# Kernel optimization log

Hardware: AMD Instinct MI355X
Metric: run time of the kernel (lower is better)

The kernel has to match this reference:

```python
import jax, jax.numpy as jnp
import numpy as np
import math

DIM = 1024
HEADS = 16
DIM_HEAD = 64
INNER = HEADS * DIM_HEAD
NUM_BUCKETS = 32
MAX_DISTANCE = 128


def setup_inputs() -> dict:
    key = jax.random.key(0)
    ks = jax.random.split(key, 6)
    x = jax.random.normal(ks[0], (2, 2048, DIM), dtype=jnp.float32)
    Wq = jax.random.normal(ks[1], (DIM, INNER), dtype=jnp.float32) * (DIM ** -0.5)
    Wkv = jax.random.normal(ks[2], (DIM, 2 * DIM_HEAD), dtype=jnp.float32) * (DIM ** -0.5)
    Wout = jax.random.normal(ks[3], (INNER, DIM), dtype=jnp.float32) * (INNER ** -0.5)
    bout = jnp.zeros((DIM,), dtype=jnp.float32)
    rel_emb = jax.random.normal(ks[4], (NUM_BUCKETS, HEADS), dtype=jnp.float32) * 0.02
    return {"x": x, "Wq": Wq, "Wkv": Wkv, "Wout": Wout, "bout": bout, "rel_emb": rel_emb}


def _relative_position_bucket(rel_pos, num_buckets=NUM_BUCKETS, max_distance=MAX_DISTANCE):
    # rel_pos: [i, j] int32, k_pos - q_pos
    n = jnp.maximum(-rel_pos, 0)
    max_exact = num_buckets // 2
    is_small = n < max_exact
    n_safe = jnp.maximum(n, 1)  # avoid log(0); masked by is_small anyway
    val_if_large = max_exact + (
        jnp.log(n_safe.astype(jnp.float32) / max_exact)
        / math.log(max_distance / max_exact)
        * (num_buckets - max_exact)
    ).astype(jnp.int32)
    val_if_large = jnp.minimum(val_if_large, num_buckets - 1)
    return jnp.where(is_small, n, val_if_large)


def reference(x, Wq, Wkv, Wout, bout, rel_emb):
    b, n, _ = x.shape
    scale = DIM_HEAD ** -0.5
    bias_scale = DIM_HEAD ** 0.5

    q = (x @ Wq).reshape(b, n, HEADS, DIM_HEAD).transpose(0, 2, 1, 3) * scale  # [b,h,n,d]
    kv = x @ Wkv  # [b,n,2d]
    k, v = kv[..., :DIM_HEAD], kv[..., DIM_HEAD:]  # shared single-head K/V [b,n,d]

    sim = jnp.einsum('bhid,bjd->bhij', q, k)

    # T5 relative position bias
    pos = jnp.arange(n, dtype=jnp.int32)
    rel_pos = pos[None, :] - pos[:, None]  # [i,j] = k_pos - q_pos
    rp_bucket = _relative_position_bucket(rel_pos)
    bias = rel_emb[rp_bucket]  # [i,j,h]
    sim = sim + jnp.transpose(bias, (2, 0, 1))[None] * bias_scale

    # causal mask: mask strictly-upper triangle
    causal_mask = jnp.triu(jnp.ones((n, n), dtype=bool), k=1)
    neg = jnp.finfo(sim.dtype).max
    sim = jnp.where(causal_mask[None, None], -neg, sim)

    attn = jax.nn.softmax(sim, axis=-1)
    out = jnp.einsum('bhij,bjd->bhid', attn, v)
    out = out.transpose(0, 2, 1, 3).reshape(b, n, INNER)
    return out @ Wout + bout
```

## Files before the change

kernel.cpp:

```cpp
#include <hip/hip_runtime.h>
#include <cstdint>
#include <cmath>

typedef _Float16 half8 __attribute__((ext_vector_type(8)));
typedef unsigned short ushort8 __attribute__((ext_vector_type(8)));
typedef float floatx4 __attribute__((ext_vector_type(4)));

#define VT_STRIDE 2080

__device__ __forceinline__ unsigned short f2h(float f) {
    union { _Float16 h; unsigned short u; } cv;
    cv.h = (_Float16)f;
    return cv.u;
}

__device__ __forceinline__ void gld_lds16(const unsigned short* g, unsigned short* l) {
    __builtin_amdgcn_global_load_lds(
        (const __attribute__((address_space(1))) unsigned int*)g,
        (__attribute__((address_space(3))) unsigned int*)l, 16, 0, 0);
}

__global__ void cast_x_kernel(const float* __restrict__ x, unsigned short* __restrict__ xh, int n8) {
    int idx = blockIdx.x * blockDim.x + threadIdx.x;
    if (idx >= n8) return;
    const float4* p = (const float4*)x;
    float4 a = p[idx * 2], b = p[idx * 2 + 1];
    ushort8 o;
    o[0] = f2h(a.x); o[1] = f2h(a.y); o[2] = f2h(a.z); o[3] = f2h(a.w);
    o[4] = f2h(b.x); o[5] = f2h(b.y); o[6] = f2h(b.z); o[7] = f2h(b.w);
    *(ushort8*)(xh + (size_t)idx * 8) = o;
}

__global__ void transpose_fused_kernel(const float* __restrict__ Wq, const float* __restrict__ Wkv,
                                       const float* __restrict__ Wout,
                                       unsigned short* __restrict__ Wqkvt, unsigned short* __restrict__ Wot) {
    __shared__ float tile[32][33];
    int bxi = blockIdx.x;
    const float* in; unsigned short* out; int C; int cb;
    if (bxi < 32)      { in = Wq;   out = Wqkvt;                 C = 1024; cb = bxi; }
    else if (bxi < 36) { in = Wkv;  out = Wqkvt + 1024 * 1024;   C = 128;  cb = bxi - 32; }
    else               { in = Wout; out = Wot;                   C = 1024; cb = bxi - 36; }
    int bx = cb * 32, by = blockIdx.y * 32;
    int x = threadIdx.x, y0 = threadIdx.y;
    #pragma unroll
    for (int k = 0; k < 4; k++) {
        int y = y0 + k * 8;
        tile[y][x] = in[(size_t)(by + y) * C + bx + x];
    }
    __syncthreads();
    #pragma unroll
    for (int k = 0; k < 4; k++) {
        int y = y0 + k * 8;
        out[(size_t)(bx + y) * 1024 + by + x] = f2h(tile[x][y]);
    }
}

template<int MODE>
__global__ __launch_bounds__(256) void gemm_mn(
    const unsigned short* __restrict__ A, const unsigned short* __restrict__ Bt,
    unsigned short* __restrict__ oq, unsigned short* __restrict__ ok,
    unsigned short* __restrict__ ov, float* __restrict__ of,
    const float* __restrict__ bias)
{
    __shared__ __align__(16) unsigned short As[64 * 40];
    __shared__ __align__(16) unsigned short Bs[128 * 40];
    const int K = 1024;
    int t = threadIdx.x;
    int w = t >> 6, lane = t & 63, g = lane >> 4, il = lane & 15;
    int m0 = blockIdx.y * 64, n0 = blockIdx.x * 128;
    int ar = t >> 2, ac = (t & 3) * 8;
    int br = t >> 1, bc = (t & 1) * 16;
    floatx4 acc[8] = {};
    const unsigned short* Ap = A + (size_t)(m0 + ar) * K + ac;
    const unsigned short* Bp = Bt + (size_t)(n0 + br) * K + bc;
    for (int k0 = 0; k0 < K; k0 += 32) {
        ushort8 av  = *(const ushort8*)(Ap + k0);
        ushort8 bv0 = *(const ushort8*)(Bp + k0);
        ushort8 bv1 = *(const ushort8*)(Bp + k0 + 8);
        __syncthreads();
        *(ushort8*)&As[ar * 40 + ac] = av;
        *(ushort8*)&Bs[br * 40 + bc] = bv0;
        *(ushort8*)&Bs[br * 40 + bc + 8] = bv1;
        __syncthreads();
        half8 af = *(const half8*)&As[(w * 16 + il) * 40 + g * 8];
        #pragma unroll
        for (int nt = 0; nt < 8; nt++) {
            half8 bf = *(const half8*)&Bs[(nt * 16 + il) * 40 + g * 8];
            acc[nt] = __builtin_amdgcn_mfma_f32_16x16x32_f16(af, bf, acc[nt], 0, 0, 0);
        }
    }
    #pragma unroll
    for (int nt = 0; nt < 8; nt++) {
        #pragma unroll
        for (int r = 0; r < 4; r++) {
            int row = m0 + w * 16 + 4 * g + r;
            int col = n0 + nt * 16 + il;
            float v = acc[nt][r];
            if (MODE == 0) {
                if (col < 1024) {
                    int b = row >> 11, i = row & 2047, h = col >> 6, d = col & 63;
                    oq[(size_t)((b * 16 + h) * 2048 + i) * 64 + d] = f2h(v * 0.18033688011112042f);
                } else if (col < 1088) {
                    ok[(size_t)row * 64 + (col - 1024)] = f2h(v);
                } else {
                    int b = row >> 11, j = row & 2047;
                    ov[(size_t)((b << 6) + (col - 1088)) * VT_STRIDE + j] = f2h(v);
                }
            } else {
                of[(size_t)row * 1024 + col] = v + bias[col];
            }
        }
    }
}

__global__ __launch_bounds__(256) void attn_kernel(
    const unsigned short* __restrict__ qh, const unsigned short* __restrict__ kh,
    const unsigned short* __restrict__ vt, const float* __restrict__ rel_emb,
    unsigned short* __restrict__ ob)
{
    __shared__ float bias_tab[256];
    __shared__ __align__(16) unsigned short Ks[2][64 * 64];
    __shared__ __align__(16) unsigned short Vs[64 * 64];
    __shared__ __align__(16) unsigned short Pl[64 * 72];

    int bx = 31 - blockIdx.y;
    int bh = blockIdx.x;
    int b = bh >> 4, h = bh & 15;
    int t = threadIdx.x;
    int w = t >> 6, lane = t & 63, g = lane >> 4, il = lane & 15;

    {
        int dlt = t;
        int bucket;
        if (dlt < 16) bucket = dlt;
        else {
            float lg = logf((float)dlt * 0.0625f) / 2.0794415416798357f;
            int vv = 16 + (int)(lg * 16.0f);
            bucket = vv < 31 ? vv : 31;
        }
        bias_tab[dlt] = rel_emb[bucket * 16 + h] * 11.541560327111708f;
    }
    float cb31 = rel_emb[31 * 16 + h] * 11.541560327111708f;

    const unsigned short* kbase = kh + (size_t)b * (2048 * 64);
    const unsigned short* vbase = vt + (size_t)b * (64 * VT_STRIDE);
    int prow = (w * 16 + il) * 72;

    int l8 = lane >> 3, b8 = lane & 7;
    int swz = (b8 ^ l8) * 8;
    const unsigned short* kg_base = kbase + (size_t)(w * 16 + l8) * 64 + swz;
    const unsigned short* vg_base = vbase + (size_t)(w * 16 + l8) * VT_STRIDE + swz;
    int e0 = (g ^ (il & 7)) * 8;

    int iw = bx * 64 + w * 16;
    int i_glob = iw + il;
    const unsigned short* qrow = qh + (size_t)(bh * 2048 + i_glob) * 64;
    half8 qf0 = *(const half8*)(qrow + g * 8);
    half8 qf1 = *(const half8*)(qrow + 32 + g * 8);
    floatx4 O[4] = {};
    float m_run = -1e30f, l_run = 0.0f;

    gld_lds16(kg_base,                 &Ks[0][(w * 16) * 64]);
    gld_lds16(kg_base + 8 * 64,        &Ks[0][(w * 16 + 8) * 64]);
    gld_lds16(vg_base,                 &Vs[(w * 16) * 64]);
    gld_lds16(vg_base + 8 * VT_STRIDE, &Vs[(w * 16 + 8) * 64]);

    for (int c = 0; c <= bx; c++) {
        __syncthreads();
        if (c < bx) {
            const unsigned short* kg = kg_base + (size_t)(c + 1) * 4096;
            unsigned short* kd = &Ks[(c + 1) & 1][0];
            gld_lds16(kg,          &kd[(w * 16) * 64]);
            gld_lds16(kg + 8 * 64, &kd[(w * 16 + 8) * 64]);
        }
        const unsigned short* Kc = &Ks[c & 1][0];
        int j0 = c * 64;

        floatx4 S[4] = {};
        #pragma unroll
        for (int jt = 0; jt < 4; jt++) {
            half8 k0 = *(const half8*)&Kc[jt * 1024 + il * 64 + e0];
            half8 k1 = *(const half8*)&Kc[jt * 1024 + il * 64 + (e0 ^ 32)];
            S[jt] = __builtin_amdgcn_mfma_f32_16x16x32_f16(k0, qf0, S[jt], 0, 0, 0);
            S[jt] = __builtin_amdgcn_mfma_f32_16x16x32_f16(k1, qf1, S[jt], 0, 0, 0);
        }
        half8 vf[8];
        #pragma unroll
        for (int ks = 0; ks < 2; ks++)
            #pragma unroll
            for (int dt = 0; dt < 4; dt++)
                vf[ks * 4 + dt] = *(const half8*)&Vs[dt * 1024 + il * 64 + (e0 ^ (ks * 32))];

        asm volatile("s_waitcnt lgkmcnt(0)" ::: "memory");
        __builtin_amdgcn_s_barrier();
        if (c < bx) {
            const unsigned short* vg = vg_base + (c + 1) * 64;
            gld_lds16(vg,                 &Vs[(w * 16) * 64]);
            gld_lds16(vg + 8 * VT_STRIDE, &Vs[(w * 16 + 8) * 64]);
        }

        float s[16];
        if (c + 3 <= bx) {
            #pragma unroll
            for (int q2 = 0; q2 < 16; q2++) s[q2] = S[q2 >> 2][q2 & 3] + cb31;
        } else if (c < bx) {
            #pragma unroll
            for (int jt = 0; jt < 4; jt++)
                #pragma unroll
                for (int r = 0; r < 4; r++)
                    s[jt * 4 + r] = S[jt][r] + bias_tab[i_glob - (j0 + jt * 16 + 4 * g + r)];
        } else {
            #pragma unroll
            for (int jt = 0; jt < 4; jt++) {
                #pragma unroll
                for (int r = 0; r < 4; r++) {
                    int delta = i_glob - (j0 + jt * 16 + 4 * g + r);
                    int di = delta > 0 ? delta : 0;
                    s[jt * 4 + r] = (delta >= 0) ? (S[jt][r] + bias_tab[di]) : -1e30f;
                }
            }
        }
        float m8[8];
        #pragma unroll
        for (int q2 = 0; q2 < 8; q2++) m8[q2] = fmaxf(s[q2], s[q2 + 8]);
        #pragma unroll
        for (int q2 = 0; q2 < 4; q2++) m8[q2] = fmaxf(m8[q2], m8[q2 + 4]);
        float mx = fmaxf(fmaxf(m8[0], m8[1]), fmaxf(m8[2], m8[3]));
        mx = fmaxf(mx, __shfl_xor(mx, 16));
        mx = fmaxf(mx, __shfl_xor(mx, 32));
        float m_new = fmaxf(m_run, mx);
        float alpha = __builtin_amdgcn_exp2f(m_run - m_new);
        float p[16];
        #pragma unroll
        for (int q2 = 0; q2 < 16; q2++) p[q2] = __builtin_amdgcn_exp2f(s[q2] - m_new);
        float ps[8];
        #pragma unroll
        for (int q2 = 0; q2 < 8; q2++) ps[q2] = p[q2] + p[q2 + 8];
        #pragma unroll
        for (int q2 = 0; q2 < 4; q2++) ps[q2] += ps[q2 + 4];
        float psum = (ps[0] + ps[1]) + (ps[2] + ps[3]);
        psum += __shfl_xor(psum, 16);
        psum += __shfl_xor(psum, 32);
        l_run = l_run * alpha + psum;
        m_run = m_new;
        float arow[4];
        #pragma unroll
        for (int r = 0; r < 4; r++) arow[r] = __shfl(alpha, 4 * g + r);
        #pragma unroll
        for (int dt = 0; dt < 4; dt++)
            #pragma unroll
            for (int r = 0; r < 4; r++) O[dt][r] *= arow[r];
        #pragma unroll
        for (int jt = 0; jt < 4; jt++) {
            uint2 u;
            u.x = (unsigned int)f2h(p[jt * 4 + 0]) | ((unsigned int)f2h(p[jt * 4 + 1]) << 16);
            u.y = (unsigned int)f2h(p[jt * 4 + 2]) | ((unsigned int)f2h(p[jt * 4 + 3]) << 16);
            *(uint2*)&Pl[prow + jt * 16 + 4 * g] = u;
        }
        #pragma unroll
        for (int ks = 0; ks < 2; ks++) {
            half8 pf = *(const half8*)&Pl[prow + ks * 32 + g * 8];
            #pragma unroll
            for (int dt = 0; dt < 4; dt++)
                O[dt] = __builtin_amdgcn_mfma_f32_16x16x32_f16(pf, vf[ks * 4 + dt], O[dt], 0, 0, 0);
        }
    }
    float inv[4];
    #pragma unroll
    for (int r = 0; r < 4; r++) inv[r] = 1.0f / __shfl(l_run, 4 * g + r);
    #pragma unroll
    for (int dt = 0; dt < 4; dt++) {
        #pragma unroll
        for (int r = 0; r < 4; r++) {
            int i = iw + 4 * g + r;
            int d = dt * 16 + il;
            ob[(size_t)(b * 2048 + i) * 1024 + h * 64 + d] = f2h(O[dt][r] * inv[r]);
        }
    }
}

extern "C" void kernel_launch(void* const* d_in, const int* in_sizes, int n_in,
                              void* d_out, int out_size, void* d_ws, size_t ws_size,
                              hipStream_t stream) {
    const float* x    = (const float*)d_in[0];
    const float* Wq   = (const float*)d_in[1];
    const float* Wkv  = (const float*)d_in[2];
    const float* Wout = (const float*)d_in[3];
    const float* bout = (const float*)d_in[4];
    const float* rel  = (const float*)d_in[5];
    float* out = (float*)d_out;

    unsigned short* ws    = (unsigned short*)d_ws;
    unsigned short* xh    = ws;
    unsigned short* qh    = xh + 4194304;
    unsigned short* kh    = qh + 4194304;
    unsigned short* vt    = kh + 262144;
    unsigned short* Wqkvt = vt + 2 * 64 * VT_STRIDE;
    unsigned short* Wot   = Wqkvt + 1179648;
    unsigned short* ob    = xh;

    cast_x_kernel<<<2048, 256, 0, stream>>>(x, xh, 524288);
    transpose_fused_kernel<<<dim3(68, 32), dim3(32, 8), 0, stream>>>(Wq, Wkv, Wout, Wqkvt, Wot);
    gemm_mn<0><<<dim3(9, 64), 256, 0, stream>>>(xh, Wqkvt, qh, kh, vt, nullptr, nullptr);
    attn_kernel<<<dim3(32, 32), 256, 0, stream>>>(qh, kh, vt, rel, ob);
    gemm_mn<2><<<dim3(8, 64), 256, 0, stream>>>(ob, Wot, nullptr, nullptr, nullptr, out, bout);
}
```

Before: 186.0 us.

## Rewrite GEMM with 128x128 tiles, async LDS loads, double buffering and swizzle

```diff
diff --git a/kernel.cpp b/kernel.cpp
--- a/kernel.cpp
+++ b/kernel.cpp
@@ -62,52 +62,78 @@
     unsigned short* __restrict__ ov, float* __restrict__ of,
     const float* __restrict__ bias)
 {
-    __shared__ __align__(16) unsigned short As[64 * 40];
-    __shared__ __align__(16) unsigned short Bs[128 * 40];
+    __shared__ __align__(16) unsigned short As[2][128 * 64];
+    __shared__ __align__(16) unsigned short Bs[2][128 * 64];
     const int K = 1024;
     int t = threadIdx.x;
     int w = t >> 6, lane = t & 63, g = lane >> 4, il = lane & 15;
-    int m0 = blockIdx.y * 64, n0 = blockIdx.x * 128;
-    int ar = t >> 2, ac = (t & 3) * 8;
-    int br = t >> 1, bc = (t & 1) * 16;
-    floatx4 acc[8] = {};
-    const unsigned short* Ap = A + (size_t)(m0 + ar) * K + ac;
-    const unsigned short* Bp = Bt + (size_t)(n0 + br) * K + bc;
-    for (int k0 = 0; k0 < K; k0 += 32) {
-        ushort8 av  = *(const ushort8*)(Ap + k0);
-        ushort8 bv0 = *(const ushort8*)(Bp + k0);
-        ushort8 bv1 = *(const ushort8*)(Bp + k0 + 8);
+    int wr = w >> 1, wc = w & 1;
+    int m0 = blockIdx.y * 128, n0 = blockIdx.x * 128;
+
+    int l8 = lane >> 3, b8 = lane & 7;
+    int swz = (b8 ^ l8) * 8;
+    const unsigned short* Ag = A  + (size_t)(m0 + w * 32 + l8) * K + swz;
+    const unsigned short* Bg = Bt + (size_t)(n0 + w * 32 + l8) * K + swz;
+    int e0 = (g ^ (il & 7)) * 8;
+
+    floatx4 acc[4][4] = {};
+
+    #pragma unroll
+    for (int q = 0; q < 4; q++) {
+        gld_lds16(Ag + (size_t)(q * 8) * K, &As[0][(w * 32 + q * 8) * 64]);
+        gld_lds16(Bg + (size_t)(q * 8) * K, &Bs[0][(w * 32 + q * 8) * 64]);
+    }
+
+    int cb = 0;
+    for (int k0 = 0; k0 < K; k0 += 64, cb ^= 1) {
         __syncthreads();
-        *(ushort8*)&As[ar * 40 + ac] = av;
-        *(ushort8*)&Bs[br * 40 + bc] = bv0;
-        *(ushort8*)&Bs[br * 40 + bc + 8] = bv1;
-        __syncthreads();
-        half8 af = *(const half8*)&As[(w * 16 + il) * 40 + g * 8];
-        #pragma unroll
-        for (int nt = 0; nt < 8; nt++) {
-            half8 bf = *(const half8*)&Bs[(nt * 16 + il) * 40 + g * 8];
-            acc[nt] = __builtin_amdgcn_mfma_f32_16x16x32_f16(af, bf, acc[nt], 0, 0, 0);
-        }
-    }
-    #pragma unroll
-    for (int nt = 0; nt < 8; nt++) {
-        #pragma unroll
-        for (int r = 0; r < 4; r++) {
-            int row = m0 + w * 16 + 4 * g + r;
-            int col = n0 + nt * 16 + il;
-            float v = acc[nt][r];
-            if (MODE == 0) {
-                if (col < 1024) {
-                    int b = row >> 11, i = row & 2047, h = col >> 6, d = col & 63;
-                    oq[(size_t)((b * 16 + h) * 2048 + i) * 64 + d] = f2h(v * 0.18033688011112042f);
-                } else if (col < 1088) {
-                    ok[(size_t)row * 64 + (col - 1024)] = f2h(v);
+        if (k0 + 64 < K) {
+            #pragma unroll
+            for (int q = 0; q < 4; q++) {
+                gld_lds16(Ag + (size_t)(q * 8) * K + k0 + 64, &As[cb ^ 1][(w * 32 + q * 8) * 64]);
+                gld_lds16(Bg + (size_t)(q * 8) * K + k0 + 64, &Bs[cb ^ 1][(w * 32 + q * 8) * 64]);
+            }
+        }
+        const unsigned short* Ac = &As[cb][0];
+        const unsigned short* Bc = &Bs[cb][0];
+        #pragma unroll
+        for (int ks = 0; ks < 2; ks++) {
+            half8 a[4];
+            #pragma unroll
+            for (int mt = 0; mt < 4; mt++)
+                a[mt] = *(const half8*)&Ac[(wr * 64 + mt * 16 + il) * 64 + (e0 ^ (ks * 32))];
+            #pragma unroll
+            for (int nt = 0; nt < 4; nt++) {
+                half8 b = *(const half8*)&Bc[(wc * 64 + nt * 16 + il) * 64 + (e0 ^ (ks * 32))];
+                #pragma unroll
+                for (int mt = 0; mt < 4; mt++)
+                    acc[mt][nt] = __builtin_amdgcn_mfma_f32_16x16x32_f16(a[mt], b, acc[mt][nt], 0, 0, 0);
+            }
+        }
+    }
+
+    #pragma unroll
+    for (int mt = 0; mt < 4; mt++) {
+        #pragma unroll
+        for (int nt = 0; nt < 4; nt++) {
+            #pragma unroll
+            for (int r = 0; r < 4; r++) {
+                int row = m0 + wr * 64 + mt * 16 + 4 * g + r;
+                int col = n0 + wc * 64 + nt * 16 + il;
+                float v = acc[mt][nt][r];
+                if (MODE == 0) {
+                    if (col < 1024) {
+                        int b = row >> 11, i = row & 2047, h = col >> 6, d = col & 63;
+                        oq[(size_t)((b * 16 + h) * 2048 + i) * 64 + d] = f2h(v * 0.18033688011112042f);
+                    } else if (col < 1088) {
+                        ok[(size_t)row * 64 + (col - 1024)] = f2h(v);
+                    } else {
+                        int b = row >> 11, j = row & 2047;
+                        ov[(size_t)((b << 6) + (col - 1088)) * VT_STRIDE + j] = f2h(v);
+                    }
                 } else {
-                    int b = row >> 11, j = row & 2047;
-                    ov[(size_t)((b << 6) + (col - 1088)) * VT_STRIDE + j] = f2h(v);
+                    of[(size_t)row * 1024 + col] = v + bias[col];
                 }
-            } else {
-                of[(size_t)row * 1024 + col] = v + bias[col];
             }
         }
     }
@@ -301,7 +327,7 @@
 
     cast_x_kernel<<<2048, 256, 0, stream>>>(x, xh, 524288);
     transpose_fused_kernel<<<dim3(68, 32), dim3(32, 8), 0, stream>>>(Wq, Wkv, Wout, Wqkvt, Wot);
-    gemm_mn<0><<<dim3(9, 64), 256, 0, stream>>>(xh, Wqkvt, qh, kh, vt, nullptr, nullptr);
+    gemm_mn<0><<<dim3(9, 32), 256, 0, stream>>>(xh, Wqkvt, qh, kh, vt, nullptr, nullptr);
     attn_kernel<<<dim3(32, 32), 256, 0, stream>>>(qh, kh, vt, rel, ob);
-    gemm_mn<2><<<dim3(8, 64), 256, 0, stream>>>(ob, Wot, nullptr, nullptr, nullptr, out, bout);
-}
+    gemm_mn<2><<<dim3(8, 32), 256, 0, stream>>>(ob, Wot, nullptr, nullptr, nullptr, out, bout);
+}
```

Measured after the change: 175.1 us. 1.06x faster.
